# Kernel optimization log

Hardware: AMD Instinct MI355X
Metric: run time of the kernel (lower is better)

Reference implementation:

```python
import jax, jax.numpy as jnp
import numpy as np

BETA = 1.0  # init_kwargs beta

B, D, N = 8, 3, 4096
LATENT = 256

def setup_inputs() -> dict:
    key = jax.random.key(0)
    k1, k2, k3, k4 = jax.random.split(key, 4)
    return {
        "recon_x": jax.random.normal(k1, (B, D, N), dtype=jnp.float32),
        "x": jax.random.normal(k2, (B, D, N), dtype=jnp.float32),
        "mu": jax.random.normal(k3, (B, LATENT), dtype=jnp.float32),
        "logvar": jax.random.normal(k4, (B, LATENT), dtype=jnp.float32),
    }

def _chamfer(xc, yc):
    # xc, yc: [B, D, N] channels-first point clouds -> [B, N, D]
    xp = jnp.swapaxes(xc, 2, 1)  # [B, N, D]
    yp = jnp.swapaxes(yc, 2, 1)  # [B, M, D]
    # squared L2 pairwise distances via gram expansion (avoids [B,N,M,D] intermediate)
    x2 = jnp.sum(xp * xp, axis=-1)               # [B, N]
    y2 = jnp.sum(yp * yp, axis=-1)               # [B, M]
    xy = jnp.einsum("bnd,bmd->bnm", xp, yp)      # [B, N, M]
    dist = x2[:, :, None] + y2[:, None, :] - 2.0 * xy  # [B, N, M]
    min_x = jnp.min(dist, axis=2)  # [B, N] nearest y for each x
    min_y = jnp.min(dist, axis=1)  # [B, M] nearest x for each y
    return jnp.mean(min_x) + jnp.mean(min_y)

def _kl(mu, logvar):
    kld = -0.5 * jnp.sum(1.0 + logvar - mu * mu - jnp.exp(logvar))
    return kld / mu.shape[0]

def reference(recon_x, x, mu, logvar):
    recon_loss = _chamfer(recon_x, x)
    kld_loss = _kl(mu, logvar)
    total_loss = recon_loss + BETA * kld_loss
    return (total_loss, recon_loss, kld_loss)
```

## Files before the change

kernel.cpp:

```cpp
#include <hip/hip_runtime.h>
#include <math.h>

#define BB 8
#define NN 4096
#define LATENT 256

#define THREADS 256
#define QPAIRS 8
#define CSPLIT 32
#define TT (NN / CSPLIT)
#define NSLOTS (2 * BB * NN)
#define BLOCKS_X (2 * BB)

__device__ __forceinline__ float min3f(float a, float b, float c) {
    float d;
    asm("v_min3_f32 %0, %1, %2, %3" : "=v"(d) : "v"(a), "v"(b), "v"(c));
    return d;
}

__device__ __forceinline__ float2 dist_pk(float2 cxy, float2 czw,
                                          float2 qx, float2 qy, float2 qz) {
    float2 t;
    asm("v_pk_fma_f32 %0, %1, %2, %1 op_sel:[0,0,1] op_sel_hi:[0,1,1]"
        : "=v"(t) : "v"(czw), "v"(qz));
    asm("v_pk_fma_f32 %0, %1, %2, %0 op_sel:[1,0,0] op_sel_hi:[1,1,1]"
        : "+v"(t) : "v"(cxy), "v"(qy));
    asm("v_pk_fma_f32 %0, %1, %2, %0 op_sel:[0,0,0] op_sel_hi:[0,1,1]"
        : "+v"(t) : "v"(cxy), "v"(qx));
    return t;
}

__global__ __launch_bounds__(THREADS)
void chamfer_stage1(const float* __restrict__ recon,
                    const float* __restrict__ x,
                    float* __restrict__ partial,
                    unsigned* __restrict__ counter)
{
    __shared__ float4 ly[TT];

    const int bx  = blockIdx.x;
    const int c   = blockIdx.y;
    const int dir = bx >> 3;
    const int b   = bx & 7;
    const int tid = threadIdx.x;

    if (bx == 0 && c == 0 && tid == 0) *counter = 0u;

    const float* cloud = (dir ? recon : x) + (size_t)b * 3 * NN;
    const float* query = (dir ? x : recon) + (size_t)b * 3 * NN;

    for (int i = tid; i < TT; i += THREADS) {
        int m = c * TT + i;
        float y0 = cloud[m];
        float y1 = cloud[NN + m];
        float y2 = cloud[2 * NN + m];
        ly[i] = make_float4(-2.0f * y0, -2.0f * y1, -2.0f * y2,
                            y0 * y0 + y1 * y1 + y2 * y2);
    }
    __syncthreads();

    float2 qx[QPAIRS], qy[QPAIRS], qz[QPAIRS];
    float mn0[QPAIRS], mn1[QPAIRS];
#pragma unroll
    for (int p = 0; p < QPAIRS; ++p) {
        int ql = p * THREADS + tid;
        int qh = ql + 2048;
        qx[p] = make_float2(query[ql],          query[qh]);
        qy[p] = make_float2(query[NN + ql],     query[NN + qh]);
        qz[p] = make_float2(query[2 * NN + ql], query[2 * NN + qh]);
        mn0[p] = 3.4e38f;
        mn1[p] = 3.4e38f;
    }

#pragma unroll 2
    for (int j = 0; j < TT; j += 2) {
        float4 A = ly[j];
        float4 B = ly[j + 1];
        float2 Axy = make_float2(A.x, A.y), Azw = make_float2(A.z, A.w);
        float2 Bxy = make_float2(B.x, B.y), Bzw = make_float2(B.z, B.w);
#pragma unroll
        for (int p = 0; p < QPAIRS; ++p) {
            float2 ta = dist_pk(Axy, Azw, qx[p], qy[p], qz[p]);
            float2 tb = dist_pk(Bxy, Bzw, qx[p], qy[p], qz[p]);
            mn0[p] = min3f(mn0[p], ta.x, tb.x);
            mn1[p] = min3f(mn1[p], ta.y, tb.y);
        }
    }

    float* dst = partial + (size_t)c * NSLOTS + dir * (BB * NN) + b * NN;
#pragma unroll
    for (int p = 0; p < QPAIRS; ++p) {
        int ql = p * THREADS + tid;
        int qh = ql + 2048;
        float sx0 = fmaf(qx[p].x, qx[p].x, fmaf(qy[p].x, qy[p].x, qz[p].x * qz[p].x));
        float sx1 = fmaf(qx[p].y, qx[p].y, fmaf(qy[p].y, qy[p].y, qz[p].y * qz[p].y));
        dst[ql] = sx0 + mn0[p];
        dst[qh] = sx1 + mn1[p];
    }
}

__global__ __launch_bounds__(THREADS)
void chamfer_stage2(const float* __restrict__ partial,
                    const float* __restrict__ mu,
                    const float* __restrict__ logvar,
                    float* __restrict__ sums,
                    unsigned* __restrict__ counter,
                    float* __restrict__ out)
{
    __shared__ float red[4];
    __shared__ float redA[4];
    __shared__ float redB[4];
    __shared__ int amLast;

    const int tid = threadIdx.x;
    const int bid = blockIdx.x;
    const int gq  = bid * THREADS + tid;

    float m0 = partial[gq];
    float m1 = partial[(size_t)1 * NSLOTS + gq];
    for (int cc = 2; cc < CSPLIT; cc += 2) {
        float a = partial[(size_t)cc * NSLOTS + gq];
        float b = partial[(size_t)(cc + 1) * NSLOTS + gq];
        m0 = fminf(m0, a);
        m1 = fminf(m1, b);
    }
    float v = fminf(m0, m1);

    for (int off = 32; off > 0; off >>= 1)
        v += __shfl_down(v, off);
    if ((tid & 63) == 0) red[tid >> 6] = v;
    __syncthreads();

    if (tid == 0) {
        float tot = red[0] + red[1] + red[2] + red[3];
        __hip_atomic_store(&sums[bid], tot, __ATOMIC_RELEASE, __HIP_MEMORY_SCOPE_AGENT);
        unsigned old = __hip_atomic_fetch_add(counter, 1u, __ATOMIC_ACQ_REL, __HIP_MEMORY_SCOPE_AGENT);
        amLast = (old == 255u);
    }
    __syncthreads();
    if (!amLast) return;

    float s = __hip_atomic_load(&sums[tid], __ATOMIC_ACQUIRE, __HIP_MEMORY_SCOPE_AGENT);

    float kl = 0.0f;
    for (int i = tid; i < BB * LATENT; i += THREADS) {
        float m  = mu[i];
        float lv = logvar[i];
        kl += 1.0f + lv - m * m - expf(lv);
    }

    for (int off = 32; off > 0; off >>= 1) {
        s  += __shfl_down(s, off);
        kl += __shfl_down(kl, off);
    }
    if ((tid & 63) == 0) { redA[tid >> 6] = s; redB[tid >> 6] = kl; }
    __syncthreads();
    if (tid == 0) {
        float recon = (redA[0] + redA[1] + redA[2] + redA[3]) / (float)(BB * NN);
        float kld   = -0.5f * (redB[0] + redB[1] + redB[2] + redB[3]) / (float)BB;
        out[0] = recon + kld;
        out[1] = recon;
        out[2] = kld;
    }
}

extern "C" void kernel_launch(void* const* d_in, const int* in_sizes, int n_in,
                              void* d_out, int out_size, void* d_ws, size_t ws_size,
                              hipStream_t stream)
{
    const float* recon  = (const float*)d_in[0];
    const float* x      = (const float*)d_in[1];
    const float* mu     = (const float*)d_in[2];
    const float* logvar = (const float*)d_in[3];
    float* out = (float*)d_out;

    float*    partial = (float*)d_ws;
    float*    sums    = partial + (size_t)CSPLIT * NSLOTS;
    unsigned* counter = (unsigned*)(sums + 256);

    dim3 g1(BLOCKS_X, CSPLIT);
    chamfer_stage1<<<g1, THREADS, 0, stream>>>(recon, x, partial, counter);
    chamfer_stage2<<<NSLOTS / THREADS, THREADS, 0, stream>>>(partial, mu, logvar,
                                                             sums, counter, out);
}
```

Before: 40.05 us.

## Use scalar FMAs with 16 contiguous queries per thread and finer cloud split

The distance loop drops the inline-asm packed FMA path and uses scalar fmaf chains. Each thread now handles 16 contiguous queries, loaded and stored as float4. The cloud is split into 64 chunks instead of 32, and a launch-bounds occupancy hint is added, so more blocks run with a smaller shared tile. The aim is fewer, wider memory accesses and more parallel blocks, at the cost of losing packed-math throughput and doubling the partial-minimum buffer that stage 2 must write and read.

```diff
diff --git a/kernel.cpp b/kernel.cpp
--- a/kernel.cpp
+++ b/kernel.cpp
@@ -6,8 +6,8 @@
 #define LATENT 256
 
 #define THREADS 256
-#define QPAIRS 8
-#define CSPLIT 32
+#define NQ 16
+#define CSPLIT 64
 #define TT (NN / CSPLIT)
 #define NSLOTS (2 * BB * NN)
 #define BLOCKS_X (2 * BB)
@@ -18,19 +18,7 @@
     return d;
 }
 
-__device__ __forceinline__ float2 dist_pk(float2 cxy, float2 czw,
-                                          float2 qx, float2 qy, float2 qz) {
-    float2 t;
-    asm("v_pk_fma_f32 %0, %1, %2, %1 op_sel:[0,0,1] op_sel_hi:[0,1,1]"
-        : "=v"(t) : "v"(czw), "v"(qz));
-    asm("v_pk_fma_f32 %0, %1, %2, %0 op_sel:[1,0,0] op_sel_hi:[1,1,1]"
-        : "+v"(t) : "v"(cxy), "v"(qy));
-    asm("v_pk_fma_f32 %0, %1, %2, %0 op_sel:[0,0,0] op_sel_hi:[0,1,1]"
-        : "+v"(t) : "v"(cxy), "v"(qx));
-    return t;
-}
-
-__global__ __launch_bounds__(THREADS)
+__global__ __launch_bounds__(THREADS, 4)
 void chamfer_stage1(const float* __restrict__ recon,
                     const float* __restrict__ x,
                     float* __restrict__ partial,
@@ -49,53 +37,54 @@
     const float* cloud = (dir ? recon : x) + (size_t)b * 3 * NN;
     const float* query = (dir ? x : recon) + (size_t)b * 3 * NN;
 
-    for (int i = tid; i < TT; i += THREADS) {
-        int m = c * TT + i;
+    if (tid < TT) {
+        int m = c * TT + tid;
         float y0 = cloud[m];
         float y1 = cloud[NN + m];
         float y2 = cloud[2 * NN + m];
-        ly[i] = make_float4(-2.0f * y0, -2.0f * y1, -2.0f * y2,
-                            y0 * y0 + y1 * y1 + y2 * y2);
+        ly[tid] = make_float4(-2.0f * y0, -2.0f * y1, -2.0f * y2,
+                              y0 * y0 + y1 * y1 + y2 * y2);
     }
     __syncthreads();
 
-    float2 qx[QPAIRS], qy[QPAIRS], qz[QPAIRS];
-    float mn0[QPAIRS], mn1[QPAIRS];
+    const float4* q4x = (const float4*)(query);
+    const float4* q4y = (const float4*)(query + NN);
+    const float4* q4z = (const float4*)(query + 2 * NN);
+
+    float qx[NQ], qy[NQ], qz[NQ], mn[NQ];
 #pragma unroll
-    for (int p = 0; p < QPAIRS; ++p) {
-        int ql = p * THREADS + tid;
-        int qh = ql + 2048;
-        qx[p] = make_float2(query[ql],          query[qh]);
-        qy[p] = make_float2(query[NN + ql],     query[NN + qh]);
-        qz[p] = make_float2(query[2 * NN + ql], query[2 * NN + qh]);
-        mn0[p] = 3.4e38f;
-        mn1[p] = 3.4e38f;
+    for (int g = 0; g < 4; ++g) {
+        float4 vx = q4x[g * 256 + tid];
+        float4 vy = q4y[g * 256 + tid];
+        float4 vz = q4z[g * 256 + tid];
+        qx[4*g+0] = vx.x; qx[4*g+1] = vx.y; qx[4*g+2] = vx.z; qx[4*g+3] = vx.w;
+        qy[4*g+0] = vy.x; qy[4*g+1] = vy.y; qy[4*g+2] = vy.z; qy[4*g+3] = vy.w;
+        qz[4*g+0] = vz.x; qz[4*g+1] = vz.y; qz[4*g+2] = vz.z; qz[4*g+3] = vz.w;
     }
+#pragma unroll
+    for (int k = 0; k < NQ; ++k) mn[k] = 3.4e38f;
 
 #pragma unroll 2
     for (int j = 0; j < TT; j += 2) {
         float4 A = ly[j];
         float4 B = ly[j + 1];
-        float2 Axy = make_float2(A.x, A.y), Azw = make_float2(A.z, A.w);
-        float2 Bxy = make_float2(B.x, B.y), Bzw = make_float2(B.z, B.w);
 #pragma unroll
-        for (int p = 0; p < QPAIRS; ++p) {
-            float2 ta = dist_pk(Axy, Azw, qx[p], qy[p], qz[p]);
-            float2 tb = dist_pk(Bxy, Bzw, qx[p], qy[p], qz[p]);
-            mn0[p] = min3f(mn0[p], ta.x, tb.x);
-            mn1[p] = min3f(mn1[p], ta.y, tb.y);
+        for (int k = 0; k < NQ; ++k) {
+            float tA = fmaf(qx[k], A.x, fmaf(qy[k], A.y, fmaf(qz[k], A.z, A.w)));
+            float tB = fmaf(qx[k], B.x, fmaf(qy[k], B.y, fmaf(qz[k], B.z, B.w)));
+            mn[k] = min3f(mn[k], tA, tB);
         }
     }
 
-    float* dst = partial + (size_t)c * NSLOTS + dir * (BB * NN) + b * NN;
+    float4* dst = (float4*)(partial + (size_t)c * NSLOTS + dir * (BB * NN) + b * NN);
 #pragma unroll
-    for (int p = 0; p < QPAIRS; ++p) {
-        int ql = p * THREADS + tid;
-        int qh = ql + 2048;
-        float sx0 = fmaf(qx[p].x, qx[p].x, fmaf(qy[p].x, qy[p].x, qz[p].x * qz[p].x));
-        float sx1 = fmaf(qx[p].y, qx[p].y, fmaf(qy[p].y, qy[p].y, qz[p].y * qz[p].y));
-        dst[ql] = sx0 + mn0[p];
-        dst[qh] = sx1 + mn1[p];
+    for (int g = 0; g < 4; ++g) {
+        float4 r;
+        r.x = fmaf(qx[4*g+0], qx[4*g+0], fmaf(qy[4*g+0], qy[4*g+0], qz[4*g+0]*qz[4*g+0])) + mn[4*g+0];
+        r.y = fmaf(qx[4*g+1], qx[4*g+1], fmaf(qy[4*g+1], qy[4*g+1], qz[4*g+1]*qz[4*g+1])) + mn[4*g+1];
+        r.z = fmaf(qx[4*g+2], qx[4*g+2], fmaf(qy[4*g+2], qy[4*g+2], qz[4*g+2]*qz[4*g+2])) + mn[4*g+2];
+        r.w = fmaf(qx[4*g+3], qx[4*g+3], fmaf(qy[4*g+3], qy[4*g+3], qz[4*g+3]*qz[4*g+3])) + mn[4*g+3];
+        dst[g * 256 + tid] = r;
     }
 }
 
```

After: 47.50 us. +18.6%, slower.
